# Optimization experiments

Measured on AMD Instinct MI355X. Metric: run time of the kernel, lower is better.

Reference implementation:

```python
import jax, jax.numpy as jnp
import numpy as np

B, S, D, H, DK, DFF = 4, 1024, 1024, 16, 64, 4096
EPS = 1e-5


def _layernorm(x, w, b):
    mu = jnp.mean(x, axis=-1, keepdims=True)
    var = jnp.mean((x - mu) ** 2, axis=-1, keepdims=True)
    return (x - mu) / jnp.sqrt(var + EPS) * w + b


def setup_inputs() -> dict:
    root = jax.random.key(0)
    ks = jax.random.split(root, 16)
    g = lambda k, shape, s=0.02: (jax.random.normal(k, shape, dtype=jnp.float32) * s)
    return {
        "mask": 1,
        "query": jax.random.normal(ks[0], (B, S, D), dtype=jnp.float32),
        "key": jax.random.normal(ks[1], (B, S, D), dtype=jnp.float32),
        "values": jax.random.normal(ks[2], (B, S, D), dtype=jnp.float32),
        "Wq": g(ks[3], (D, D)), "bq": jnp.zeros((D,), jnp.float32),
        "Wk": g(ks[4], (D, D)), "bk": jnp.zeros((D,), jnp.float32),
        "Wv": g(ks[5], (D, D)), "bv": jnp.zeros((D,), jnp.float32),
        "Wo": g(ks[6], (D, D)), "bo": jnp.zeros((D,), jnp.float32),
        "gammas": g(ks[7], (H, 1, 1), 0.5),
        "ln1_w": jnp.ones((D,), jnp.float32), "ln1_b": jnp.zeros((D,), jnp.float32),
        "W1": g(ks[8], (DFF, D)), "b1": jnp.zeros((DFF,), jnp.float32),
        "W2": g(ks[9], (D, DFF)), "b2": jnp.zeros((D,), jnp.float32),
        "ln2_w": jnp.ones((D,), jnp.float32), "ln2_b": jnp.zeros((D,), jnp.float32),
    }


def _forward(mask, query, key, values, Wq, bq, Wk, bk, Wv, bv, Wo, bo, gammas,
             ln1_w, ln1_b, W1, b1, W2, b2, ln2_w, ln2_b):
    # mask is a static Python int (the triu offset)
    allowed = jnp.triu(jnp.ones((S, S), dtype=jnp.float32), k=mask) == 0  # [S,S] bool

    def proj(x, W, b):  # [B,S,D] -> [B,H,S,DK]
        return (x @ W.T + b).reshape(B, S, H, DK).transpose(0, 2, 1, 3)

    q = proj(query, Wq, bq)
    k = proj(key, Wk, bk)
    v = proj(values, Wv, bv)

    scores = jnp.einsum('bhid,bhjd->bhij', q, k) / jnp.sqrt(jnp.float32(DK))

    # distance-decay factor, computed without gradient (torch.no_grad + detach)
    def dist_block(sc):
        sc_ = jax.nn.softmax(sc, axis=-1) * allowed.astype(sc.dtype)
        distcum = jnp.cumsum(sc_, axis=-1)
        disttot = jnp.sum(sc_, axis=-1, keepdims=True)
        idx = jnp.arange(S, dtype=jnp.float32)
        pos = jnp.abs(idx[None, :] - idx[:, None])[None, None]  # [1,1,S,S]
        return jnp.sqrt(jnp.clip((disttot - distcum) * pos, 0.0, None))
    dist_scores = jax.lax.stop_gradient(dist_block(scores))

    gamma = -jax.nn.softplus(gammas)[None]  # [1,H,1,1]
    total_effect = jnp.clip(jnp.exp(dist_scores * gamma), 1e-5, 1e5)
    scores = scores * total_effect
    scores = jnp.where(allowed, scores, jnp.float32(-1e20))
    attn = jax.nn.softmax(scores, axis=-1)
    if mask == 0:  # zero_pad first query row
        attn = attn.at[:, :, 0, :].set(0.0)

    out = jnp.einsum('bhij,bhjd->bhid', attn, v)
    concat = out.transpose(0, 2, 1, 3).reshape(B, S, D)
    attn_out = concat @ Wo.T + bo

    x = _layernorm(query + attn_out, ln1_w, ln1_b)
    ffn = jax.nn.relu(x @ W1.T + b1) @ W2.T + b2
    return _layernorm(x + ffn, ln2_w, ln2_b)


def reference(mask, query, key, values, Wq, bq, Wk, bk, Wv, bv, Wo, bo, gammas,
              ln1_w, ln1_b, W1, b1, W2, b2, ln2_w, ln2_b):
    return _forward(mask, query, key, values, Wq, bq, Wk, bk, Wv, bv, Wo, bo,
                    gammas, ln1_w, ln1_b, W1, b1, W2, b2, ln2_w, ln2_b)
```

## Files before the change

### kernel.cpp

```cpp
#include <hip/hip_runtime.h>
#include <hip/hip_bf16.h>
#include <math.h>

#define BB   4
#define SS   1024
#define DDIM 1024
#define HH   16
#define DKK  64
#define DFFF 4096
#define JC2  64

typedef __attribute__((ext_vector_type(8))) short short8;
typedef __attribute__((ext_vector_type(4))) float f32x4;
typedef unsigned short ushort;

__device__ __forceinline__ ushort f2bf(float f) {
    unsigned int u = __float_as_uint(f);
    unsigned int r = (u + 0x7FFFu + ((u >> 16) & 1u)) >> 16;
    return (ushort)r;
}
__device__ __forceinline__ short8 pack8(float4 f0, float4 f1) {
    short8 s;
    s[0] = (short)f2bf(f0.x); s[1] = (short)f2bf(f0.y);
    s[2] = (short)f2bf(f0.z); s[3] = (short)f2bf(f0.w);
    s[4] = (short)f2bf(f1.x); s[5] = (short)f2bf(f1.y);
    s[6] = (short)f2bf(f1.z); s[7] = (short)f2bf(f1.w);
    return s;
}

#define GLD16(g, l) __builtin_amdgcn_global_load_lds( \
    (const __attribute__((address_space(1))) unsigned int*)(g), \
    (__attribute__((address_space(3))) unsigned int*)(l), 16, 0, 0)

__device__ __forceinline__ float fexp2(float x) { return __builtin_amdgcn_exp2f(x); }

__device__ __forceinline__ float scan16(float x) {
    x += __int_as_float(__builtin_amdgcn_update_dpp(0, __float_as_int(x), 0x111, 0xF, 0xF, true));
    x += __int_as_float(__builtin_amdgcn_update_dpp(0, __float_as_int(x), 0x112, 0xF, 0xF, true));
    x += __int_as_float(__builtin_amdgcn_update_dpp(0, __float_as_int(x), 0x114, 0xF, 0xF, true));
    x += __int_as_float(__builtin_amdgcn_update_dpp(0, __float_as_int(x), 0x118, 0xF, 0xF, true));
    return x;
}
__device__ __forceinline__ float bcast15(float x) {
    return __int_as_float(__builtin_amdgcn_ds_swizzle(__float_as_int(x), 0x1F0));
}

__device__ __forceinline__ float block_reduce_sum(float v, float* red, int tid) {
#pragma unroll
    for (int off = 32; off; off >>= 1) v += __shfl_xor(v, off);
    __syncthreads();
    if ((tid & 63) == 0) red[tid >> 6] = v;
    __syncthreads();
    return red[0] + red[1] + red[2] + red[3];
}

struct CvtArgs { const float* s[6]; ushort* d[6]; unsigned int n[6]; };
__global__ __launch_bounds__(256) void convert_bf(CvtArgs a) {
    const int seg = blockIdx.y;
    size_t idx = ((size_t)blockIdx.x * 256 + threadIdx.x) * 8;
    if (idx >= a.n[seg]) return;
    const float* s = a.s[seg];
    float4 f0 = *(const float4*)(s + idx);
    float4 f1 = *(const float4*)(s + idx + 4);
    *(short8*)(a.d[seg] + idx) = pack8(f0, f1);
}

template <int BM, typename TC, bool RELU, bool BIAS, bool CVTA>
__device__ __forceinline__ void gemm_core(const void* __restrict__ Av, int lda,
                                          const ushort* __restrict__ Bm, int ldb,
                                          const float* __restrict__ bias,
                                          TC* __restrict__ C, int N, int Klen,
                                          int bm, int bn) {
    constexpr int MT = BM / 32;
    constexpr int PA = BM / 32;
    __shared__ ushort A_s[BM * 64];
    __shared__ ushort B_s[128 * 64];
    const int t = threadIdx.x;
    const int lane = t & 63, w = t >> 6;
    const int wr = w >> 1, wc = w & 1;
    const int fm = lane & 15, fq = lane >> 4;
    const int srl = lane >> 3;
    const int sg8 = ((lane & 7) ^ srl) << 3;

    f32x4 acc[MT][4];
#pragma unroll
    for (int mt = 0; mt < MT; mt++)
#pragma unroll
        for (int nt = 0; nt < 4; nt++) acc[mt][nt] = (f32x4){0.f, 0.f, 0.f, 0.f};

    for (int kt = 0; kt < Klen; kt += 64) {
        __syncthreads();
        if constexpr (CVTA) {
            const float* Af = (const float*)Av;
#pragma unroll
            for (int p = 0; p < PA; ++p) {
                int rowg = (w * PA + p) * 8;
                const float* src = Af + (size_t)(bm + rowg + srl) * lda + kt + sg8;
                float4 f0 = *(const float4*)(src);
                float4 f1 = *(const float4*)(src + 4);
                *(short8*)&A_s[(rowg + srl) * 64 + ((lane & 7) << 3)] = pack8(f0, f1);
            }
        } else {
            const ushort* A = (const ushort*)Av;
#pragma unroll
            for (int p = 0; p < PA; ++p) {
                int rowg = (w * PA + p) * 8;
                GLD16(A + (size_t)(bm + rowg + srl) * lda + kt + sg8, &A_s[rowg * 64]);
            }
        }
#pragma unroll
        for (int p = 0; p < 4; ++p) {
            int rowg = (w * 4 + p) * 8;
            GLD16(Bm + (size_t)(bn + rowg + srl) * ldb + kt + sg8, &B_s[rowg * 64]);
        }
        __syncthreads();

        short8 av[2][MT], bv[2][4];
        const int sw = fm & 7;
#pragma unroll
        for (int mt = 0; mt < MT; ++mt) {
            int row = wr * (BM / 2) + mt * 16 + fm;
#pragma unroll
            for (int ks = 0; ks < 2; ++ks)
                av[ks][mt] = *(const short8*)&A_s[row * 64 + (((ks * 4 + fq) ^ sw) << 3)];
        }
#pragma unroll
        for (int nt = 0; nt < 4; ++nt) {
            int row = wc * 64 + nt * 16 + fm;
#pragma unroll
            for (int ks = 0; ks < 2; ++ks)
                bv[ks][nt] = *(const short8*)&B_s[row * 64 + (((ks * 4 + fq) ^ sw) << 3)];
        }
#pragma unroll
        for (int ks = 0; ks < 2; ++ks)
#pragma unroll
            for (int mt = 0; mt < MT; ++mt)
#pragma unroll
                for (int nt = 0; nt < 4; ++nt)
                    acc[mt][nt] = __builtin_amdgcn_mfma_f32_16x16x32_bf16(
                        av[ks][mt], bv[ks][nt], acc[mt][nt], 0, 0, 0);
    }

#pragma unroll
    for (int mt = 0; mt < MT; mt++) {
        int row0 = bm + wr * (BM / 2) + mt * 16 + fq * 4;
#pragma unroll
        for (int nt = 0; nt < 4; nt++) {
            int col = bn + wc * 64 + nt * 16 + fm;
            float bsv = BIAS ? bias[col] : 0.f;
#pragma unroll
            for (int r = 0; r < 4; r++) {
                float val = acc[mt][nt][r] + bsv;
                if (RELU) val = fmaxf(val, 0.f);
                if constexpr (sizeof(TC) == 4)
                    ((float*)C)[(size_t)(row0 + r) * N + col] = val;
                else
                    ((ushort*)C)[(size_t)(row0 + r) * N + col] = f2bf(val);
            }
        }
    }
}

template <int BM, typename TC, bool RELU>
__global__ __launch_bounds__(256, 2) void gemm_bf(const ushort* __restrict__ A,
                                                  const ushort* __restrict__ Bm,
                                                  const float* __restrict__ bias,
                                                  TC* __restrict__ C,
                                                  int N, int K) {
    gemm_core<BM, TC, RELU, true, false>(A, K, Bm, K, bias, C, N, K,
                                         blockIdx.y * BM, blockIdx.x * 128);
}

struct QkvArgs { const float* A[3]; const ushort* B[3]; const float* bias[3]; ushort* C[3]; };
__global__ __launch_bounds__(256, 2) void gemm_qkv(QkvArgs qa) {
    const int g = blockIdx.z;
    gemm_core<128, ushort, false, true, true>(qa.A[g], DDIM, qa.B[g], DDIM,
                                              qa.bias[g], qa.C[g], DDIM, DDIM,
                                              blockIdx.y * 128, blockIdx.x * 128);
}

struct SkArgs { const ushort* A; const ushort* Bm; float* C0; float* C1; int lda; int Klen; };
__global__ __launch_bounds__(256, 2) void gemm_splitk(SkArgs s) {
    const int z = blockIdx.z;
    float* C = z ? s.C1 : s.C0;
    const int koff = z * s.Klen;
    gemm_core<128, float, false, false, false>(s.A + koff, s.lda, s.Bm + koff, s.lda,
                                               nullptr, C, DDIM, s.Klen,
                                               blockIdx.y * 128, blockIdx.x * 128);
}

__global__ __launch_bounds__(256, 4) void attn_flash(
    const ushort* __restrict__ Q, const ushort* __restrict__ Kg,
    const ushort* __restrict__ Vg, const float* __restrict__ gammas,
    const int* __restrict__ maskp, ushort* __restrict__ out) {
    __shared__ short QP[64 * 72];
    __shared__ short KsD[2][64 * 64];
    __shared__ short Vts[64 * 72];

    const int t = threadIdx.x;
    const int lane = t & 63, w = t >> 6;
    const int col = lane & 15;
    const int quad = lane >> 4;
    const int srl = lane >> 3;
    const int sg8 = ((lane & 7) ^ srl) << 3;
    const int swk = col & 7;

    const int bid = blockIdx.x;
    const int xcls = bid & 7;
    const int m = bid >> 3;
    const int bh = xcls + ((m & 7) << 3);
    const int itr = m >> 3;
    const int yy = itr & 3, jj = itr >> 2;
    const int it = (((yy + jj) & 3) << 2) + ((2 * yy + jj) & 3);
    const int h = bh & (HH - 1);
    const int b = bh >> 4;
    const int i0 = it * 64;
    const int mask = *maskp;

    const float LOG2E = 1.44269504f;
    const float SC2 = 0.125f * LOG2E;
    const float g0 = gammas[h];
    const float gnat = -((g0 > 20.f) ? g0 : log1pf(__expf(g0)));
    const float g2 = gnat * LOG2E;

    const size_t qbase = ((size_t)(b * SS + i0)) * DDIM + h * DKK;
    const size_t kvbase = ((size_t)b * SS) * DDIM + h * DKK;

#define STAGE_K(jc, kb) \
    { _Pragma("unroll") for (int p = 0; p < 2; ++p) { \
        int rowg = (w * 2 + p) * 8; \
        GLD16(Kg + kvbase + (size_t)((jc) + rowg + srl) * DDIM + sg8, \
              &KsD[kb][rowg * 64]); } }

    {
        int r = t >> 2, d0 = (t & 3) << 4;
        const ushort* gq = Q + qbase + (size_t)r * DDIM + d0;
        *(short8*)&QP[r * 72 + d0]     = *(const short8*)(gq);
        *(short8*)&QP[r * 72 + d0 + 8] = *(const short8*)(gq + 8);
        STAGE_K(0, 0);
    }
    __syncthreads();
    const short8 qa0 = *(const short8*)&QP[(w * 16 + col) * 72 + quad * 8];
    const short8 qa1 = *(const short8*)&QP[(w * 16 + col) * 72 + 32 + quad * 8];

    float m1[4], su[4], smT[4], gi4[4];
    int lim4[4];
#pragma unroll
    for (int r = 0; r < 4; ++r) {
        m1[r] = -3.4e38f; su[r] = 0.f; smT[r] = 0.f;
        int gi = i0 + w * 16 + quad * 4 + r;
        gi4[r] = (float)gi;
        lim4[r] = gi + mask;
    }

    int buf = 0;
    for (int ck = 0; ck < SS / JC2; ++ck) {
        const int jc = ck * JC2;
        const int njc = ((ck + 1) & 15) * JC2;
        STAGE_K(njc, buf ^ 1);
#pragma unroll
        for (int g = 0; g < 4; ++g) {
            const short* Kr = &KsD[buf][(g * 16 + col) * 64];
            short8 kb0 = *(const short8*)&Kr[(quad ^ swk) << 3];
            short8 kb1 = *(const short8*)&Kr[((4 + quad) ^ swk) << 3];
            f32x4 c = (f32x4){0.f, 0.f, 0.f, 0.f};
            c = __builtin_amdgcn_mfma_f32_16x16x32_bf16(qa0, kb0, c, 0, 0, 0);
            c = __builtin_amdgcn_mfma_f32_16x16x32_bf16(qa1, kb1, c, 0, 0, 0);
            int j = jc + g * 16 + col;
#pragma unroll
            for (int r = 0; r < 4; ++r) {
                float s2 = c[r] * SC2;
                m1[r] = fmaxf(m1[r], s2);
                float ev = fexp2(s2);
                su[r] += ev;
                smT[r] += (j < lim4[r]) ? ev : 0.f;
            }
        }
        __syncthreads();
        buf ^= 1;
    }
#pragma unroll
    for (int off = 1; off < 16; off <<= 1) {
#pragma unroll
        for (int r = 0; r < 4; ++r) {
            m1[r] = fmaxf(m1[r], __shfl_xor(m1[r], off, 16));
            su[r] += __shfl_xor(su[r], off, 16);
            smT[r] += __shfl_xor(smT[r], off, 16);
        }
    }
    float lse2[4], smTn[4], ms2[4];
#pragma unroll
    for (int r = 0; r < 4; ++r) {
        lse2[r] = __log2f(su[r]);
        smTn[r] = smT[r] / su[r];
        ms2[r]  = fmaxf(m1[r], 0.f);
    }

    const int nck2 = min(SS / JC2, max(1, (i0 + 62 + mask) / 64 + 1));

    float l2[4], carry[4];
    f32x4 o[4];
#pragma unroll
    for (int r = 0; r < 4; ++r) { l2[r] = 0.f; carry[r] = 0.f; }
#pragma unroll
    for (int dg = 0; dg < 4; ++dg) o[dg] = (f32x4){0.f, 0.f, 0.f, 0.f};

    short* Pw = &QP[w * 16 * 72];

    for (int ck = 0; ck < nck2; ++ck) {
        const int jc = ck * JC2;
        if (ck + 1 < nck2) STAGE_K((ck + 1) * JC2, buf ^ 1);
        {
            int j = t & 63, dq = t >> 6, d0 = dq * 16;
            const ushort* gv = Vg + kvbase + (size_t)(jc + j) * DDIM + d0;
            short8 v0 = *(const short8*)(gv);
            short8 v1 = *(const short8*)(gv + 8);
#pragma unroll
            for (int k = 0; k < 8; ++k) {
                Vts[(d0 + k) * 72 + j]     = v0[k];
                Vts[(d0 + 8 + k) * 72 + j] = v1[k];
            }
        }

#pragma unroll
        for (int g = 0; g < 4; ++g) {
            const short* Kr = &KsD[buf][(g * 16 + col) * 64];
            short8 kb0 = *(const short8*)&Kr[(quad ^ swk) << 3];
            short8 kb1 = *(const short8*)&Kr[((4 + quad) ^ swk) << 3];
            f32x4 c = (f32x4){0.f, 0.f, 0.f, 0.f};
            c = __builtin_amdgcn_mfma_f32_16x16x32_bf16(qa0, kb0, c, 0, 0, 0);
            c = __builtin_amdgcn_mfma_f32_16x16x32_bf16(qa1, kb1, c, 0, 0, 0);
            const int j = jc + g * 16 + col;
            const float jf = (float)j;
#pragma unroll
            for (int r = 0; r < 4; ++r) {
                float s2 = c[r] * SC2;
                float pj = fexp2(s2 - lse2[r]);
                float incl = (j < lim4[r]) ? pj : 0.f;
                incl = scan16(incl);
                float tot = bcast15(incl);
                float Cc = carry[r] + incl;
                carry[r] += tot;
                float pos = fabsf(jf - gi4[r]);
                float d2 = fmaxf((smTn[r] - Cc) * pos, 0.f);
                float dist = __builtin_amdgcn_sqrtf(d2);
                float eff = fmaxf(fexp2(g2 * dist), 1e-5f);
                float pe = fexp2(s2 * eff - ms2[r]);
                float p = (j < lim4[r]) ? pe : 0.f;
                l2[r] += p;
                Pw[(quad * 4 + r) * 72 + g * 16 + col] = (short)f2bf(p);
            }
        }
        __syncthreads();
#pragma unroll
        for (int kg = 0; kg < 2; ++kg) {
            short8 pa = *(const short8*)&Pw[col * 72 + kg * 32 + quad * 8];
#pragma unroll
            for (int dg = 0; dg < 4; ++dg) {
                short8 vb = *(const short8*)&Vts[(dg * 16 + col) * 72 + kg * 32 + quad * 8];
                o[dg] = __builtin_amdgcn_mfma_f32_16x16x32_bf16(pa, vb, o[dg], 0, 0, 0);
            }
        }
        __syncthreads();
        buf ^= 1;
    }

#pragma unroll
    for (int off = 1; off < 16; off <<= 1)
#pragma unroll
        for (int r = 0; r < 4; ++r) l2[r] += __shfl_xor(l2[r], off, 16);

#pragma unroll
    for (int r = 0; r < 4; ++r) {
        int irow = i0 + w * 16 + quad * 4 + r;
        float scl = 1.f / l2[r];
        if (mask == 0 && irow == 0) scl = 0.f;
        size_t base = ((size_t)(b * SS) + irow) * DDIM + h * DKK;
#pragma unroll
        for (int dg = 0; dg < 4; ++dg)
            out[base + dg * 16 + col] = f2bf(o[dg][r] * scl);
    }
#undef STAGE_K
}

template <bool WB>
__global__ __launch_bounds__(256) void add_ln(const float* __restrict__ R,
                                              const float* __restrict__ Y0,
                                              const float* __restrict__ Y1,
                                              const float* __restrict__ gb,
                                              const float* __restrict__ w,
                                              const float* __restrict__ bb,
                                              float* __restrict__ out,
                                              ushort* __restrict__ obf) {
    const int row = blockIdx.x;
    const int tid = threadIdx.x;
    __shared__ float red[4];
    const size_t base = (size_t)row * DDIM;
    const int i4 = tid * 4;
    float4 a  = *(const float4*)(R  + base + i4);
    float4 y0 = *(const float4*)(Y0 + base + i4);
    float4 y1 = *(const float4*)(Y1 + base + i4);
    float4 g  = *(const float4*)(gb + i4);
    float4 x;
    x.x = a.x + y0.x + y1.x + g.x;
    x.y = a.y + y0.y + y1.y + g.y;
    x.z = a.z + y0.z + y1.z + g.z;
    x.w = a.w + y0.w + y1.w + g.w;
    float s  = (x.x + x.y) + (x.z + x.w);
    float s2 = (x.x * x.x + x.y * x.y) + (x.z * x.z + x.w * x.w);
    s = block_reduce_sum(s, red, tid);
    s2 = block_reduce_sum(s2, red, tid);
    const float mu = s * (1.f / DDIM);
    const float var = s2 * (1.f / DDIM) - mu * mu;
    const float rstd = rsqrtf(var + 1e-5f);
    float4 wv = *(const float4*)(w + i4);
    float4 bv = *(const float4*)(bb + i4);
    float4 v;
    v.x = (x.x - mu) * rstd * wv.x + bv.x;
    v.y = (x.y - mu) * rstd * wv.y + bv.y;
    v.z = (x.z - mu) * rstd * wv.z + bv.z;
    v.w = (x.w - mu) * rstd * wv.w + bv.w;
    *(float4*)(out + base + i4) = v;
    if (WB) {
        ushort4 o4;
        o4.x = f2bf(v.x); o4.y = f2bf(v.y); o4.z = f2bf(v.z); o4.w = f2bf(v.w);
        *(ushort4*)(obf + base + i4) = o4;
    }
}

extern "C" void kernel_launch(void* const* d_in, const int* in_sizes, int n_in,
                              void* d_out, int out_size, void* d_ws, size_t ws_size,
                              hipStream_t stream) {
    const int*   maskp  = (const int*)d_in[0];
    const float* query  = (const float*)d_in[1];
    const float* key    = (const float*)d_in[2];
    const float* values = (const float*)d_in[3];
    const float* Wq = (const float*)d_in[4];
    const float* bq = (const float*)d_in[5];
    const float* Wk = (const float*)d_in[6];
    const float* bk = (const float*)d_in[7];
    const float* Wv = (const float*)d_in[8];
    const float* bv = (const float*)d_in[9];
    const float* Wo = (const float*)d_in[10];
    const float* bo = (const float*)d_in[11];
    const float* gammas = (const float*)d_in[12];
    const float* ln1w = (const float*)d_in[13];
    const float* ln1b = (const float*)d_in[14];
    const float* W1 = (const float*)d_in[15];
    const float* b1 = (const float*)d_in[16];
    const float* W2 = (const float*)d_in[17];
    const float* b2 = (const float*)d_in[18];
    const float* ln2w = (const float*)d_in[19];
    const float* ln2b = (const float*)d_in[20];

    const int M = BB * SS;
    const size_t MB = 1048576;
    char* wsb = (char*)d_ws;
    ushort* Wq_bf = (ushort*)(wsb + 0 * MB);
    ushort* Wk_bf = (ushort*)(wsb + 8 * MB);
    ushort* Wv_bf = (ushort*)(wsb + 16 * MB);
    ushort* Wo_bf = (ushort*)(wsb + 24 * MB);
    ushort* W1_bf = (ushort*)(wsb + 32 * MB);
    ushort* W2_bf = (ushort*)(wsb + 40 * MB);
    ushort* Qb    = (ushort*)(wsb + 72 * MB);
    ushort* Kb    = (ushort*)(wsb + 80 * MB);
    ushort* Vb    = (ushort*)(wsb + 88 * MB);
    ushort* ATTb  = (ushort*)(wsb + 96 * MB);
    float*  Ysp0  = (float*)(wsb + 104 * MB);
    float*  Ysp1  = (float*)(wsb + 120 * MB);
    float*  xf    = (float*)(wsb + 48 * MB);
    ushort* x_bf  = (ushort*)(wsb + 64 * MB);
    ushort* hidden= (ushort*)(wsb + 72 * MB);

    dim3 blk(256);

    const unsigned int N4M = 4u * 1024 * 1024, N1M = 1024 * 1024;
    CvtArgs ca;
    ca.s[0] = Wq; ca.s[1] = Wk; ca.s[2] = Wv; ca.s[3] = Wo;
    ca.s[4] = W1; ca.s[5] = W2;
    ca.d[0] = Wq_bf; ca.d[1] = Wk_bf; ca.d[2] = Wv_bf; ca.d[3] = Wo_bf;
    ca.d[4] = W1_bf; ca.d[5] = W2_bf;
    ca.n[0] = N1M; ca.n[1] = N1M; ca.n[2] = N1M; ca.n[3] = N1M;
    ca.n[4] = N4M; ca.n[5] = N4M;
    convert_bf<<<dim3(2048, 6), blk, 0, stream>>>(ca);

    QkvArgs qa;
    qa.A[0] = query; qa.A[1] = key; qa.A[2] = values;
    qa.B[0] = Wq_bf; qa.B[1] = Wk_bf; qa.B[2] = Wv_bf;
    qa.bias[0] = bq; qa.bias[1] = bk; qa.bias[2] = bv;
    qa.C[0] = Qb; qa.C[1] = Kb; qa.C[2] = Vb;
    gemm_qkv<<<dim3(8, 32, 3), blk, 0, stream>>>(qa);

    attn_flash<<<dim3(BB * HH * 16), blk, 0, stream>>>(Qb, Kb, Vb, gammas, maskp, ATTb);

    {
        SkArgs s; s.A = ATTb; s.Bm = Wo_bf; s.C0 = Ysp0; s.C1 = Ysp1;
        s.lda = DDIM; s.Klen = DDIM / 2;
        gemm_splitk<<<dim3(8, 32, 2), blk, 0, stream>>>(s);
    }

    add_ln<true><<<dim3(M), blk, 0, stream>>>(query, Ysp0, Ysp1, bo, ln1w, ln1b, xf, x_bf);

    gemm_bf<128, ushort, true><<<dim3(32, 32), blk, 0, stream>>>(x_bf, W1_bf, b1, hidden, DFFF, DDIM);

    {
        SkArgs s; s.A = hidden; s.Bm = W2_bf; s.C0 = Ysp0; s.C1 = Ysp1;
        s.lda = DFFF; s.Klen = DFFF / 2;
        gemm_splitk<<<dim3(8, 32, 2), blk, 0, stream>>>(s);
    }

    add_ln<false><<<dim3(M), blk, 0, stream>>>(xf, Ysp0, Ysp1, b2, ln2w, ln2b, (float*)d_out, nullptr);
}
```

Baseline: 402.0 us.

## Overlap Wo/W1/W2 conversion with QKV GEMM and split FFN2 GEMM 4-way

The standalone weight-conversion launch now converts only Wq/Wk/Wv. The Wo, W1 and W2 conversions move into an extra z-slice of the QKV GEMM grid, so they run alongside the projection blocks. The second FFN GEMM (K=4096) goes from a 2-way to a 4-way split-K, which doubles its block count to raise occupancy. The final add+LayerNorm then sums four partials. The cost is more fp32 partial traffic, and the two extra partial buffers reuse workspace regions that earlier held the Wq/Wk bf16 weights.

```diff
diff --git a/kernel.cpp b/kernel.cpp
--- a/kernel.cpp
+++ b/kernel.cpp
@@ -54,11 +54,10 @@
     return red[0] + red[1] + red[2] + red[3];
 }
 
-struct CvtArgs { const float* s[6]; ushort* d[6]; unsigned int n[6]; };
+struct CvtArgs { const float* s[3]; ushort* d[3]; };
 __global__ __launch_bounds__(256) void convert_bf(CvtArgs a) {
     const int seg = blockIdx.y;
     size_t idx = ((size_t)blockIdx.x * 256 + threadIdx.x) * 8;
-    if (idx >= a.n[seg]) return;
     const float* s = a.s[seg];
     float4 f0 = *(const float4*)(s + idx);
     float4 f1 = *(const float4*)(s + idx + 4);
@@ -171,9 +170,26 @@
                                          blockIdx.y * BM, blockIdx.x * 128);
 }
 
-struct QkvArgs { const float* A[3]; const ushort* B[3]; const float* bias[3]; ushort* C[3]; };
+struct QkvArgs {
+    const float* A[3]; const ushort* B[3]; const float* bias[3]; ushort* C[3];
+    const float* cs[3]; ushort* cd[3]; unsigned int cn[3];
+};
 __global__ __launch_bounds__(256, 2) void gemm_qkv(QkvArgs qa) {
     const int g = blockIdx.z;
+    if (g == 3) {
+        const unsigned int gtid = (blockIdx.y * 8 + blockIdx.x) * 256 + threadIdx.x;
+        const unsigned int total = qa.cn[0] + qa.cn[1] + qa.cn[2];
+        for (unsigned int c = gtid; c < total; c += 65536) {
+            unsigned int off = c; int seg = 0;
+            if (off >= qa.cn[0]) { off -= qa.cn[0]; seg = 1; }
+            if (seg == 1 && off >= qa.cn[1]) { off -= qa.cn[1]; seg = 2; }
+            const float* s = qa.cs[seg] + (size_t)off * 8;
+            float4 f0 = *(const float4*)(s);
+            float4 f1 = *(const float4*)(s + 4);
+            *(short8*)(qa.cd[seg] + (size_t)off * 8) = pack8(f0, f1);
+        }
+        return;
+    }
     gemm_core<128, ushort, false, true, true>(qa.A[g], DDIM, qa.B[g], DDIM,
                                               qa.bias[g], qa.C[g], DDIM, DDIM,
                                               blockIdx.y * 128, blockIdx.x * 128);
@@ -183,9 +199,17 @@
 __global__ __launch_bounds__(256, 2) void gemm_splitk(SkArgs s) {
     const int z = blockIdx.z;
     float* C = z ? s.C1 : s.C0;
-    const int koff = z * s.Klen;
-    gemm_core<128, float, false, false, false>(s.A + koff, s.lda, s.Bm + koff, s.lda,
+    gemm_core<128, float, false, false, false>(s.A + z * s.Klen, s.lda,
+                                               s.Bm + z * s.Klen, s.lda,
                                                nullptr, C, DDIM, s.Klen,
+                                               blockIdx.y * 128, blockIdx.x * 128);
+}
+struct Sk4Args { const ushort* A; const ushort* Bm; float* C[4]; int lda; int Klen; };
+__global__ __launch_bounds__(256, 2) void gemm_splitk4(Sk4Args s) {
+    const int z = blockIdx.z;
+    gemm_core<128, float, false, false, false>(s.A + z * s.Klen, s.lda,
+                                               s.Bm + z * s.Klen, s.lda,
+                                               nullptr, s.C[z], DDIM, s.Klen,
                                                blockIdx.y * 128, blockIdx.x * 128);
 }
 
@@ -383,10 +407,12 @@
 #undef STAGE_K
 }
 
-template <bool WB>
+template <bool WB, int NY>
 __global__ __launch_bounds__(256) void add_ln(const float* __restrict__ R,
                                               const float* __restrict__ Y0,
                                               const float* __restrict__ Y1,
+                                              const float* __restrict__ Y2,
+                                              const float* __restrict__ Y3,
                                               const float* __restrict__ gb,
                                               const float* __restrict__ w,
                                               const float* __restrict__ bb,
@@ -406,6 +432,12 @@
     x.y = a.y + y0.y + y1.y + g.y;
     x.z = a.z + y0.z + y1.z + g.z;
     x.w = a.w + y0.w + y1.w + g.w;
+    if constexpr (NY == 4) {
+        float4 y2 = *(const float4*)(Y2 + base + i4);
+        float4 y3 = *(const float4*)(Y3 + base + i4);
+        x.x += y2.x + y3.x; x.y += y2.y + y3.y;
+        x.z += y2.z + y3.z; x.w += y2.w + y3.w;
+    }
     float s  = (x.x + x.y) + (x.z + x.w);
     float s2 = (x.x * x.x + x.y * x.y) + (x.z * x.z + x.w * x.w);
     s = block_reduce_sum(s, red, tid);
@@ -468,28 +500,30 @@
     ushort* ATTb  = (ushort*)(wsb + 96 * MB);
     float*  Ysp0  = (float*)(wsb + 104 * MB);
     float*  Ysp1  = (float*)(wsb + 120 * MB);
+    float*  Ysp2  = (float*)(wsb + 0 * MB);
+    float*  Ysp3  = (float*)(wsb + 16 * MB);
     float*  xf    = (float*)(wsb + 48 * MB);
     ushort* x_bf  = (ushort*)(wsb + 64 * MB);
     ushort* hidden= (ushort*)(wsb + 72 * MB);
 
     dim3 blk(256);
 
-    const unsigned int N4M = 4u * 1024 * 1024, N1M = 1024 * 1024;
     CvtArgs ca;
-    ca.s[0] = Wq; ca.s[1] = Wk; ca.s[2] = Wv; ca.s[3] = Wo;
-    ca.s[4] = W1; ca.s[5] = W2;
-    ca.d[0] = Wq_bf; ca.d[1] = Wk_bf; ca.d[2] = Wv_bf; ca.d[3] = Wo_bf;
-    ca.d[4] = W1_bf; ca.d[5] = W2_bf;
-    ca.n[0] = N1M; ca.n[1] = N1M; ca.n[2] = N1M; ca.n[3] = N1M;
-    ca.n[4] = N4M; ca.n[5] = N4M;
-    convert_bf<<<dim3(2048, 6), blk, 0, stream>>>(ca);
+    ca.s[0] = Wq; ca.s[1] = Wk; ca.s[2] = Wv;
+    ca.d[0] = Wq_bf; ca.d[1] = Wk_bf; ca.d[2] = Wv_bf;
+    convert_bf<<<dim3(512, 3), blk, 0, stream>>>(ca);
 
     QkvArgs qa;
     qa.A[0] = query; qa.A[1] = key; qa.A[2] = values;
     qa.B[0] = Wq_bf; qa.B[1] = Wk_bf; qa.B[2] = Wv_bf;
     qa.bias[0] = bq; qa.bias[1] = bk; qa.bias[2] = bv;
     qa.C[0] = Qb; qa.C[1] = Kb; qa.C[2] = Vb;
-    gemm_qkv<<<dim3(8, 32, 3), blk, 0, stream>>>(qa);
+    qa.cs[0] = Wo; qa.cs[1] = W1; qa.cs[2] = W2;
+    qa.cd[0] = Wo_bf; qa.cd[1] = W1_bf; qa.cd[2] = W2_bf;
+    qa.cn[0] = (1024u * 1024) / 8;
+    qa.cn[1] = (4096u * 1024) / 8;
+    qa.cn[2] = (4096u * 1024) / 8;
+    gemm_qkv<<<dim3(8, 32, 4), blk, 0, stream>>>(qa);
 
     attn_flash<<<dim3(BB * HH * 16), blk, 0, stream>>>(Qb, Kb, Vb, gammas, maskp, ATTb);
 
@@ -499,15 +533,18 @@
         gemm_splitk<<<dim3(8, 32, 2), blk, 0, stream>>>(s);
     }
 
-    add_ln<true><<<dim3(M), blk, 0, stream>>>(query, Ysp0, Ysp1, bo, ln1w, ln1b, xf, x_bf);
+    add_ln<true, 2><<<dim3(M), blk, 0, stream>>>(query, Ysp0, Ysp1, nullptr, nullptr,
+                                                 bo, ln1w, ln1b, xf, x_bf);
 
     gemm_bf<128, ushort, true><<<dim3(32, 32), blk, 0, stream>>>(x_bf, W1_bf, b1, hidden, DFFF, DDIM);
 
     {
-        SkArgs s; s.A = hidden; s.Bm = W2_bf; s.C0 = Ysp0; s.C1 = Ysp1;
-        s.lda = DFFF; s.Klen = DFFF / 2;
-        gemm_splitk<<<dim3(8, 32, 2), blk, 0, stream>>>(s);
-    }
-
-    add_ln<false><<<dim3(M), blk, 0, stream>>>(xf, Ysp0, Ysp1, b2, ln2w, ln2b, (float*)d_out, nullptr);
-}
+        Sk4Args s; s.A = hidden; s.Bm = W2_bf;
+        s.C[0] = Ysp0; s.C[1] = Ysp1; s.C[2] = Ysp2; s.C[3] = Ysp3;
+        s.lda = DFFF; s.Klen = DFFF / 4;
+        gemm_splitk4<<<dim3(8, 32, 4), blk, 0, stream>>>(s);
+    }
+
+    add_ln<false, 4><<<dim3(M), blk, 0, stream>>>(xf, Ysp0, Ysp1, Ysp2, Ysp3,
+                                                  b2, ln2w, ln2b, (float*)d_out, nullptr);
+}
```

After: 433.9 us. +7.9%, slower.
